# Kernel optimization log

Measured on AMD Instinct MI355X. Metric: run time of the kernel, lower is better.

The kernel has to match this reference:

```python
import jax, jax.numpy as jnp
from jax import lax
import numpy as np

B = 2
N_PER = 12000
TIMES = 16
C_IN = 4
# sparse_shape = grid_size[::-1] + [1,0,0], grid_size=[160,160,40]
S1 = (41, 160, 160)
S2 = (21, 80, 80)   # conv2: k3 s2 p1
S3 = (11, 40, 40)   # conv3: k3 s2 p1
S4 = (5, 20, 20)    # conv4: k3 s2 p(0,1,1)
SOUT = (2, 20, 20)  # conv_out: k(3,1,1) s(2,1,1) p0
# per-BN-layer channel counts, flattened into gamma/beta vectors
CH = [16, 16, 32, 32, 32, 64, 64, 64, 64, 64, 64, 128]
OFF = np.concatenate([[0], np.cumsum(CH)]).tolist()


def _downsample_coords(coords, in_shape, k, s, p):
    # spconv SparseConv3d output index rule: output j active iff some active
    # input x satisfies j*s - p <= x <= j*s - p + k - 1 within bounds.
    out_shape = np.array([(in_shape[i] + 2 * p[i] - k[i]) // s[i] + 1 for i in range(3)])
    b, xs = coords[:, :1], coords[:, 1:]
    s_arr = np.array(s)
    cand = []
    for o0 in range(k[0]):
        for o1 in range(k[1]):
            for o2 in range(k[2]):
                j = xs + np.array([p[0] - o0, p[1] - o1, p[2] - o2])
                ok = np.all(j % s_arr == 0, axis=1)
                jj = j // s_arr
                ok &= np.all((jj >= 0) & (jj < out_shape), axis=1)
                cand.append(np.concatenate([b[ok], jj[ok]], axis=1))
    return np.unique(np.concatenate(cand, axis=0), axis=0).astype(np.int32)


def _make_coords():
    rng = np.random.default_rng(0)
    ncell = S1[0] * S1[1] * S1[2]
    per = []
    for b in range(B):
        flat = rng.choice(ncell, size=N_PER, replace=False)
        z, y, x = np.unravel_index(flat, S1)
        per.append(np.stack([np.full(N_PER, b), z, y, x], axis=1))
    c1 = np.concatenate(per, axis=0).astype(np.int32)
    c2 = _downsample_coords(c1, S1, (3, 3, 3), (2, 2, 2), (1, 1, 1))
    c3 = _downsample_coords(c2, S2, (3, 3, 3), (2, 2, 2), (1, 1, 1))
    c4 = _downsample_coords(c3, S3, (3, 3, 3), (2, 2, 2), (0, 1, 1))
    c5 = _downsample_coords(c4, S4, (3, 1, 1), (2, 1, 1), (0, 0, 0))
    return c1, c2, c3, c4, c5


def _w(key, shape):
    fan_in = shape[0] * shape[1] * shape[2] * shape[3]
    return jax.random.normal(key, shape, jnp.float32) * np.float32(np.sqrt(2.0 / fan_in))


def setup_inputs():
    c1, c2, c3, c4, c5 = _make_coords()
    ks = jax.random.split(jax.random.key(0), 16)
    t = TIMES
    return {
        "voxel_features": jax.random.normal(ks[0], (c1.shape[0], C_IN), jnp.float32),
        "w_in": _w(ks[1], (3, 3, 3, C_IN, t)),
        "w1": _w(ks[2], (3, 3, 3, t, t)),
        "w2_0": _w(ks[3], (3, 3, 3, t, 2 * t)),
        "w2_1": _w(ks[4], (3, 3, 3, 2 * t, 2 * t)),
        "w2_2": _w(ks[5], (3, 3, 3, 2 * t, 2 * t)),
        "w3_0": _w(ks[6], (3, 3, 3, 2 * t, 4 * t)),
        "w3_1": _w(ks[7], (3, 3, 3, 4 * t, 4 * t)),
        "w3_2": _w(ks[8], (3, 3, 3, 4 * t, 4 * t)),
        "w4_0": _w(ks[9], (3, 3, 3, 4 * t, 4 * t)),
        "w4_1": _w(ks[10], (3, 3, 3, 4 * t, 4 * t)),
        "w4_2": _w(ks[11], (3, 3, 3, 4 * t, 4 * t)),
        "w_out": _w(ks[12], (3, 1, 1, 4 * t, 8 * t)),
        "gamma": 1.0 + 0.1 * jax.random.normal(ks[13], (sum(CH),), jnp.float32),
        "beta": 0.1 * jax.random.normal(ks[14], (sum(CH),), jnp.float32),
        "coords1": jnp.asarray(c1), "coords2": jnp.asarray(c2),
        "coords3": jnp.asarray(c3), "coords4": jnp.asarray(c4),
        "coords_out": jnp.asarray(c5),
    }


def _sp_conv(feats, in_coords, w, in_shape, out_coords, stride, padding):
    # spconv's rulebook gather->matmul->scatter over active sites computes the
    # same values as a dense conv on a zero-filled grid, read back only at the
    # active output coordinates (subm: out_coords == in_coords).
    dense = jnp.zeros((B,) + in_shape + (feats.shape[1],), feats.dtype)
    dense = dense.at[in_coords[:, 0], in_coords[:, 1], in_coords[:, 2], in_coords[:, 3]].set(feats)
    out = lax.conv_general_dilated(dense, w, window_strides=stride,
                                   padding=[(p, p) for p in padding],
                                   dimension_numbers=("NDHWC", "DHWIO", "NDHWC"))
    return out[out_coords[:, 0], out_coords[:, 1], out_coords[:, 2], out_coords[:, 3]]


def _bn_relu(x, g, b):
    # nn.BatchNorm1d(eps=1e-3) in training mode over the active voxels, + ReLU
    mu = jnp.mean(x, axis=0)
    var = jnp.mean(jnp.square(x - mu), axis=0)
    return jax.nn.relu((x - mu) * (g * lax.rsqrt(var + 1e-3)) + b)


def _forward(voxel_features, ws, gamma, beta, c1, c2, c3, c4, c5):
    layers = [
        (0, c1, S1, c1, (1, 1, 1), (1, 1, 1)),   # conv_input (subm, 4->16)
        (1, c1, S1, c1, (1, 1, 1), (1, 1, 1)),   # conv1 (subm)
        (2, c1, S1, c2, (2, 2, 2), (1, 1, 1)),   # conv2 spconv s2
        (3, c2, S2, c2, (1, 1, 1), (1, 1, 1)),
        (4, c2, S2, c2, (1, 1, 1), (1, 1, 1)),
        (5, c2, S2, c3, (2, 2, 2), (1, 1, 1)),   # conv3 spconv s2
        (6, c3, S3, c3, (1, 1, 1), (1, 1, 1)),
        (7, c3, S3, c3, (1, 1, 1), (1, 1, 1)),
        (8, c3, S3, c4, (2, 2, 2), (0, 1, 1)),   # conv4 spconv s2, pad (0,1,1)
        (9, c4, S4, c4, (1, 1, 1), (1, 1, 1)),
        (10, c4, S4, c4, (1, 1, 1), (1, 1, 1)),
        (11, c4, S4, c5, (2, 1, 1), (0, 0, 0)),  # conv_out k(3,1,1) s(2,1,1)
    ]
    x = voxel_features
    for i, ci, si, co, st, pd in layers:
        x = _sp_conv(x, ci, ws[i], si, co, st, pd)
        x = _bn_relu(x, gamma[OFF[i]:OFF[i + 1]], beta[OFF[i]:OFF[i + 1]])
    return x  # encoded_spconv_tensor features, [N_out, 8*times]


def reference(voxel_features, w_in, w1, w2_0, w2_1, w2_2, w3_0, w3_1, w3_2,
              w4_0, w4_1, w4_2, w_out, gamma, beta,
              coords1, coords2, coords3, coords4, coords_out):
    ws = [w_in, w1, w2_0, w2_1, w2_2, w3_0, w3_1, w3_2, w4_0, w4_1, w4_2, w_out]
    return _forward(voxel_features, ws, gamma, beta,
                    coords1, coords2, coords3, coords4, coords_out)
```

## Files before the change

kernel.cpp:

```cpp
#include <hip/hip_runtime.h>
#include <hip/hip_bf16.h>


typedef __attribute__((ext_vector_type(8))) short bf16x8;
typedef __attribute__((ext_vector_type(4))) short bf16x4s;
typedef __attribute__((ext_vector_type(4))) float f32x4;

typedef const __attribute__((address_space(1))) unsigned int* gas_ptr;
typedef __attribute__((address_space(3))) unsigned int* las_ptr;

__device__ __forceinline__ void dma16(const unsigned short* g, unsigned short* l) {
    __builtin_amdgcn_global_load_lds((gas_ptr)g, (las_ptr)l, 16, 0, 0);
}

__device__ __forceinline__ int xcd_swz(int wg, int nwg) {
    const int x = wg & 7, i = wg >> 3;
    const int q = nwg >> 3, r = nwg & 7;
    return (x < r ? x * (q + 1) : r * (q + 1) + (x - r) * q) + i;
}

__device__ inline unsigned short f2bf(float f) {
    unsigned u = __builtin_bit_cast(unsigned, f);
    u += 0x7FFFu + ((u >> 16) & 1u);
    return (unsigned short)(u >> 16);
}

struct ScatterArgs {
    const int* coords[4];
    int* grid[4];
    int n[4];
    int D[4], H[4], W[4];
};

__global__ __launch_bounds__(256) void scatter_grid_all(ScatterArgs a) {
    const int l = blockIdx.y;
    const int i = blockIdx.x * 256 + threadIdx.x;
    if (i >= a.n[l]) return;
    const int* c = a.coords[l] + 4 * i;
    a.grid[l][((c[0] * a.D[l] + c[1]) * a.H[l] + c[2]) * a.W[l] + c[3]] = i;
}

struct PrepArgs {
    const float* src[11];
    unsigned short* dst[11];
    int T[11], CIN[11], COUT[11], total[11];
};

__global__ __launch_bounds__(256) void prep_w_all(PrepArgs a) {
    const int l = blockIdx.y;
    const int i = blockIdx.x * 256 + threadIdx.x;
    if (i >= a.total[l]) return;
    const int COUT = a.COUT[l], CIN = a.CIN[l], T = a.T[l];
    const int co = i % COUT; const int r = i / COUT; const int ci = r % CIN; const int t = r / CIN;
    unsigned short v = (t < T) ? f2bf(a.src[l][i]) : (unsigned short)0;
    a.dst[l][((size_t)t * COUT + co) * CIN + ci] = v;
}

__global__ __launch_bounds__(256, 4) void sp_conv0(const float* __restrict__ fin,
                                                   const int* __restrict__ grid,
                                                   const int* __restrict__ oc, int n_out,
                                                   const float* __restrict__ w,
                                                   float* __restrict__ out,
                                                   int D, int H, int W) {
    const int c = threadIdx.x & 15;
    const int p = (blockIdx.x * 256 + threadIdx.x) >> 4;
    if (p >= n_out) return;
    const int b   = oc[4*p+0];
    const int iz0 = oc[4*p+1] - 1;
    const int iy0 = oc[4*p+2] - 1;
    const int ix0 = oc[4*p+3] - 1;
    const int* gb = grid + b * (D * H * W);
    float acc = 0.f;
    for (int kd = 0; kd < 3; ++kd) {
        const int iz = iz0 + kd;
        if ((unsigned)iz >= (unsigned)D) continue;
        for (int kh = 0; kh < 3; ++kh) {
            const int iy = iy0 + kh;
            if ((unsigned)iy >= (unsigned)H) continue;
            for (int kw = 0; kw < 3; ++kw) {
                const int ix = ix0 + kw;
                if ((unsigned)ix >= (unsigned)W) continue;
                const int idx = gb[(iz*H + iy)*W + ix];
                if (idx < 0) continue;
                const float4 v = *(const float4*)(fin + (size_t)idx * 4);
                const float* wp = w + (size_t)((kd*3 + kh)*3 + kw) * 64 + c;
                acc = fmaf(v.x, wp[0],  acc);
                acc = fmaf(v.y, wp[16], acc);
                acc = fmaf(v.z, wp[32], acc);
                acc = fmaf(v.w, wp[48], acc);
            }
        }
    }
    out[(size_t)p*16 + c] = acc;
}

template<int COUT>
__global__ __launch_bounds__(256, 4) void sp_conv_lds16(
    const unsigned short* __restrict__ fin, const int* __restrict__ grid,
    const int* __restrict__ oc, int n_out,
    const unsigned short* __restrict__ wt, float* __restrict__ out,
    float* __restrict__ stats,
    int D, int H, int W, int sz, int sy, int sx, int pz, int py, int px)
{
    constexpr int T  = 27;
    constexpr int BT = 4;
    constexpr int TP = 28;
    constexpr int NT = COUT/16;
    constexpr int NB = (COUT == 16) ? BT/2 : BT;

    __shared__ unsigned short Abuf[4*BT*16*16];
    __shared__ unsigned short Bbuf[BT*COUT*16];
    __shared__ float ls[2*COUT];

    const int l     = threadIdx.x & 63;
    const int w     = threadIdx.x >> 6;
    const int n     = l & 15;
    const int quad  = l >> 4;
    const int pbase = xcd_swz(blockIdx.x, gridDim.x) * 64 + w * 16;

    if (threadIdx.x < 2*COUT) ls[threadIdx.x] = 0.f;

    int idx[TP];
    if (quad == 0) {
        int pc = pbase + n;
        if (pc > n_out - 1) pc = n_out - 1;
        const int4 cc = ((const int4*)oc)[pc];
        const int* gb = grid + cc.x * (D * H * W);
        const int iz0 = cc.y * sz - pz;
        const int iy0 = cc.z * sy - py;
        const int ix0 = cc.w * sx - px;
#pragma unroll
        for (int tap = 0; tap < TP; ++tap) {
            const int te = tap < T ? tap : 0;
            const int kd = te/9, kr = te%9, kh = kr/3, kw = kr%3;
            const int iz = iz0 + kd, iy = iy0 + kh, ix = ix0 + kw;
            const bool ok = (tap < T) && (unsigned)iz < (unsigned)D &&
                            (unsigned)iy < (unsigned)H && (unsigned)ix < (unsigned)W;
            const int cz = iz < 0 ? 0 : (iz >= D ? D-1 : iz);
            const int cy = iy < 0 ? 0 : (iy >= H ? H-1 : iy);
            const int cx = ix < 0 ? 0 : (ix >= W ? W-1 : ix);
            const int g = gb[(cz*H + cy)*W + cx];
            idx[tap] = ok ? g : -1;
        }
    }

    f32x4 acc[NT];
#pragma unroll
    for (int t = 0; t < NT; ++t) acc[t] = (f32x4){0.f, 0.f, 0.f, 0.f};

    const int h  = l >> 5;
    const int m  = (l >> 1) & 15;
    const int ch = l & 1;

#pragma unroll
    for (int tb0 = 0; tb0 < TP; tb0 += BT) {
#pragma unroll
        for (int q = 0; q < BT/2; ++q) {
            const int v0 = __shfl(idx[tb0 + 2*q],     m);
            const int v1 = __shfl(idx[tb0 + 2*q + 1], m);
            const int row = h ? v1 : v0;
            const unsigned short* gp = fin + (ptrdiff_t)row*16 + ch*8;
            unsigned short* lp = Abuf + (w*BT + 2*q)*16*16;
            dma16(gp, lp);
        }
        for (int q = w; q < NB; q += 4) {
            if constexpr (COUT == 16) {
                const int tap = tb0 + 2*q + h;
                const int tw = tap < T ? tap : T;
                const unsigned short* gp = wt + ((size_t)tw*COUT + m)*16 + ch*8;
                unsigned short* lp = Bbuf + (2*q)*COUT*16;
                dma16(gp, lp);
            } else {
                const int tap = tb0 + q;
                const int tw = tap < T ? tap : T;
                const int r = l >> 1;
                const unsigned short* gp = wt + ((size_t)tw*COUT + r)*16 + ch*8;
                unsigned short* lp = Bbuf + q*COUT*16;
                dma16(gp, lp);
            }
        }
        __syncthreads();
#pragma unroll
        for (int jp = 0; jp < BT/2; ++jp) {
            const int ts = 2*jp + (quad >> 1);
            bf16x8 a = *(const bf16x8*)(Abuf + ((w*BT + ts)*16 + n)*16 + (quad & 1)*8);
#pragma unroll
            for (int t = 0; t < NT; ++t) {
                bf16x8 b = *(const bf16x8*)(Bbuf + (ts*COUT + t*16 + n)*16 + (quad & 1)*8);
                acc[t] = __builtin_amdgcn_mfma_f32_16x16x32_bf16(a, b, acc[t], 0, 0, 0);
            }
        }
        __syncthreads();
    }

#pragma unroll
    for (int t = 0; t < NT; ++t)
#pragma unroll
        for (int r = 0; r < 4; ++r) {
            const int p = pbase + quad*4 + r;
            if (p < n_out) out[(size_t)p * COUT + t*16 + n] = acc[t][r];
        }

#pragma unroll
    for (int t = 0; t < NT; ++t) {
        float s1 = 0.f, s2 = 0.f;
#pragma unroll
        for (int r = 0; r < 4; ++r) {
            const int p = pbase + quad*4 + r;
            if (p < n_out) { const float v = acc[t][r]; s1 += v; s2 += v*v; }
        }
        s1 += __shfl_xor(s1, 16); s2 += __shfl_xor(s2, 16);
        s1 += __shfl_xor(s1, 32); s2 += __shfl_xor(s2, 32);
        if (quad == 0) {
            atomicAdd(&ls[t*16 + n], s1);
            atomicAdd(&ls[COUT + t*16 + n], s2);
        }
    }
    __syncthreads();
    if (threadIdx.x < 2*COUT) atomicAdd(&stats[threadIdx.x], ls[threadIdx.x]);
}

template<int CIN, int COUT, int BT, int KD, int KH, int KW, int MB>
__global__ __launch_bounds__(256, MB) void sp_conv_lds(
    const unsigned short* __restrict__ fin, const int* __restrict__ grid,
    const int* __restrict__ oc, int n_out,
    const unsigned short* __restrict__ wt, float* __restrict__ out,
    float* __restrict__ stats,
    int D, int H, int W, int sz, int sy, int sx, int pz, int py, int px)
{
    constexpr int T    = KD*KH*KW;
    constexpr int TP   = ((T + BT - 1)/BT)*BT;
    constexpr int NT   = COUT/16;
    constexpr int S    = CIN/32;
    constexpr int LPR  = CIN/8;
    constexpr int RPD  = 64/LPR;
    constexpr int ADMA = 16/RPD;
    constexpr int BDMA = COUT/RPD;

    __shared__ unsigned short Abuf[4*BT*16*CIN];
    __shared__ unsigned short Bbuf[BT*COUT*CIN];
    __shared__ float ls[2*COUT];

    const int l     = threadIdx.x & 63;
    const int w     = threadIdx.x >> 6;
    const int n     = l & 15;
    const int quad  = l >> 4;
    const int pbase = xcd_swz(blockIdx.x, gridDim.x) * 64 + w * 16;

    if (threadIdx.x < 2*COUT) ls[threadIdx.x] = 0.f;

    int idx[TP];
    if (quad == 0) {
        int pc = pbase + n;
        if (pc > n_out - 1) pc = n_out - 1;
        const int4 cc = ((const int4*)oc)[pc];
        const int* gb = grid + cc.x * (D * H * W);
        const int iz0 = cc.y * sz - pz;
        const int iy0 = cc.z * sy - py;
        const int ix0 = cc.w * sx - px;
#pragma unroll
        for (int tap = 0; tap < TP; ++tap) {
            const int te = tap < T ? tap : 0;
            const int kd = te/(KH*KW), kr = te%(KH*KW), kh = kr/KW, kw = kr%KW;
            const int iz = iz0 + kd, iy = iy0 + kh, ix = ix0 + kw;
            const bool ok = (tap < T) && (unsigned)iz < (unsigned)D &&
                            (unsigned)iy < (unsigned)H && (unsigned)ix < (unsigned)W;
            const int cz = iz < 0 ? 0 : (iz >= D ? D-1 : iz);
            const int cy = iy < 0 ? 0 : (iy >= H ? H-1 : iy);
            const int cx = ix < 0 ? 0 : (ix >= W ? W-1 : ix);
            const int g = gb[(cz*H + cy)*W + cx];
            idx[tap] = ok ? g : -1;
        }
    }

    f32x4 acc[NT];
#pragma unroll
    for (int t = 0; t < NT; ++t) acc[t] = (f32x4){0.f, 0.f, 0.f, 0.f};

#pragma unroll
    for (int tb0 = 0; tb0 < TP; tb0 += BT) {
#pragma unroll
        for (int j = 0; j < BT; ++j) {
#pragma unroll
            for (int d = 0; d < ADMA; ++d) {
                const int m  = d*RPD + l/LPR;
                const int i0 = __shfl(idx[tb0+j], m);
                const int slot = (l % LPR) ^ (m % LPR);
                const unsigned short* gp = fin + (ptrdiff_t)i0*CIN + slot*8;
                unsigned short* lp = Abuf + ((w*BT + j)*16 + d*RPD)*CIN;
                dma16(gp, lp);
            }
        }
        for (int q = w; q < BT*BDMA; q += 4) {
            const int j = q / BDMA, d = q % BDMA;
            const int t = tb0 + j;
            const int tw = t < T ? t : T;
            const int r  = d*RPD + l/LPR;
            const int slot = (l % LPR) ^ (r % LPR);
            const unsigned short* gp = wt + ((size_t)tw*COUT + r)*CIN + slot*8;
            unsigned short* lp = Bbuf + (j*COUT + d*RPD)*CIN;
            dma16(gp, lp);
        }
        __syncthreads();
#pragma unroll
        for (int j = 0; j < BT; ++j) {
            const unsigned short* Aw = Abuf + (w*BT + j)*16*CIN;
            const unsigned short* Bw = Bbuf + j*COUT*CIN;
#pragma unroll
            for (int s = 0; s < S; ++s) {
                const int c = s*4 + quad;
                bf16x8 a = *(const bf16x8*)(Aw + n*CIN + ((c ^ (n % LPR)) * 8));
#pragma unroll
                for (int t = 0; t < NT; ++t) {
                    const int r = t*16 + n;
                    bf16x8 b = *(const bf16x8*)(Bw + r*CIN + ((c ^ (r % LPR)) * 8));
                    acc[t] = __builtin_amdgcn_mfma_f32_16x16x32_bf16(a, b, acc[t], 0, 0, 0);
                }
            }
        }
        __syncthreads();
    }

#pragma unroll
    for (int t = 0; t < NT; ++t)
#pragma unroll
        for (int r = 0; r < 4; ++r) {
            const int p = pbase + quad*4 + r;
            if (p < n_out) out[(size_t)p * COUT + t*16 + n] = acc[t][r];
        }

#pragma unroll
    for (int t = 0; t < NT; ++t) {
        float s1 = 0.f, s2 = 0.f;
#pragma unroll
        for (int r = 0; r < 4; ++r) {
            const int p = pbase + quad*4 + r;
            if (p < n_out) { const float v = acc[t][r]; s1 += v; s2 += v*v; }
        }
        s1 += __shfl_xor(s1, 16); s2 += __shfl_xor(s2, 16);
        s1 += __shfl_xor(s1, 32); s2 += __shfl_xor(s2, 32);
        if (quad == 0) {
            atomicAdd(&ls[t*16 + n], s1);
            atomicAdd(&ls[COUT + t*16 + n], s2);
        }
    }
    __syncthreads();
    if (threadIdx.x < 2*COUT) atomicAdd(&stats[threadIdx.x], ls[threadIdx.x]);
}

template<int CIN, int COUT, int BT, int MT, int MB>
__global__ __launch_bounds__(256, MB) void sp_conv_big(
    const unsigned short* __restrict__ fin, const int* __restrict__ grid,
    const int* __restrict__ oc, int n_out,
    const unsigned short* __restrict__ wt, float* __restrict__ out,
    float* __restrict__ stats,
    int D, int H, int W, int sz, int sy, int sx, int pz, int py, int px)
{
    constexpr int T    = 27;
    constexpr int TP   = ((T + BT - 1)/BT)*BT;
    constexpr int PPW  = MT*16;
    constexpr int NT   = COUT/16;
    constexpr int S    = CIN/32;
    constexpr int LPR  = CIN/8;
    constexpr int RPD  = 64/LPR;
    constexpr int ADMA = PPW/RPD;
    constexpr int BDMA = COUT/RPD;

    __shared__ unsigned short Abuf[4*BT*PPW*CIN];
    __shared__ unsigned short Bbuf[BT*COUT*CIN];
    __shared__ float ls[2*COUT];

    const int l     = threadIdx.x & 63;
    const int w     = threadIdx.x >> 6;
    const int n     = l & 15;
    const int quad  = l >> 4;
    const int wbase = xcd_swz(blockIdx.x, gridDim.x) * (4*PPW) + w * PPW;

    if (threadIdx.x < 2*COUT) ls[threadIdx.x] = 0.f;

    int idx[TP];
    {
        int pc = wbase + (l % PPW);
        if (pc > n_out - 1) pc = n_out - 1;
        const int4 cc = ((const int4*)oc)[pc];
        const int* gb = grid + cc.x * (D * H * W);
        const int iz0 = cc.y * sz - pz;
        const int iy0 = cc.z * sy - py;
        const int ix0 = cc.w * sx - px;
#pragma unroll
        for (int tap = 0; tap < TP; ++tap) {
            const int te = tap < T ? tap : 0;
            const int kd = te/9, kr = te%9, kh = kr/3, kw = kr%3;
            const int iz = iz0 + kd, iy = iy0 + kh, ix = ix0 + kw;
            const bool ok = (tap < T) && (unsigned)iz < (unsigned)D &&
                            (unsigned)iy < (unsigned)H && (unsigned)ix < (unsigned)W;
            const int cz = iz < 0 ? 0 : (iz >= D ? D-1 : iz);
            const int cy = iy < 0 ? 0 : (iy >= H ? H-1 : iy);
            const int cx = ix < 0 ? 0 : (ix >= W ? W-1 : ix);
            const int g = gb[(cz*H + cy)*W + cx];
            idx[tap] = ok ? g : -1;
        }
    }

    f32x4 acc[MT][NT];
#pragma unroll
    for (int mt = 0; mt < MT; ++mt)
#pragma unroll
        for (int t = 0; t < NT; ++t) acc[mt][t] = (f32x4){0.f, 0.f, 0.f, 0.f};

#pragma unroll
    for (int tb0 = 0; tb0 < TP; tb0 += BT) {
#pragma unroll
        for (int j = 0; j < BT; ++j) {
#pragma unroll
            for (int d = 0; d < ADMA; ++d) {
                const int r  = d*RPD + l/LPR;
                const int i0 = __shfl(idx[tb0+j], r);
                const int slot = (l % LPR) ^ (r % LPR);
                const unsigned short* gp = fin + (ptrdiff_t)i0*CIN + slot*8;
                unsigned short* lp = Abuf + ((w*BT + j)*PPW + d*RPD)*CIN;
                dma16(gp, lp);
            }
        }
        for (int q = w; q < BT*BDMA; q += 4) {
            const int j = q / BDMA, d = q % BDMA;
            const int t = tb0 + j;
            const int tw = t < T ? t : T;
            const int r  = d*RPD + l/LPR;
            const int slot = (l % LPR) ^ (r % LPR);
            const unsigned short* gp = wt + ((size_t)tw*COUT + r)*CIN + slot*8;
            unsigned short* lp = Bbuf + (j*COUT + d*RPD)*CIN;
            dma16(gp, lp);
        }
        __syncthreads();
#pragma unroll
        for (int j = 0; j < BT; ++j) {
            const unsigned short* Aw = Abuf + (w*BT + j)*PPW*CIN;
            const unsigned short* Bw = Bbuf + j*COUT*CIN;
#pragma unroll
            for (int s = 0; s < S; ++s) {
                const int c = s*4 + quad;
                bf16x8 bfr[NT];
#pragma unroll
                for (int t = 0; t < NT; ++t) {
                    const int r = t*16 + n;
                    bfr[t] = *(const bf16x8*)(Bw + r*CIN + ((c ^ (r % LPR)) * 8));
                }
#pragma unroll
                for (int mt = 0; mt < MT; ++mt) {
                    bf16x8 a = *(const bf16x8*)(Aw + (mt*16 + n)*CIN + ((c ^ (n % LPR)) * 8));
#pragma unroll
                    for (int t = 0; t < NT; ++t)
                        acc[mt][t] = __builtin_amdgcn_mfma_f32_16x16x32_bf16(a, bfr[t], acc[mt][t], 0, 0, 0);
                }
            }
        }
        __syncthreads();
    }

#pragma unroll
    for (int mt = 0; mt < MT; ++mt)
#pragma unroll
        for (int t = 0; t < NT; ++t)
#pragma unroll
            for (int r = 0; r < 4; ++r) {
                const int p = wbase + mt*16 + quad*4 + r;
                if (p < n_out) out[(size_t)p * COUT + t*16 + n] = acc[mt][t][r];
            }

#pragma unroll
    for (int t = 0; t < NT; ++t) {
        float s1 = 0.f, s2 = 0.f;
#pragma unroll
        for (int mt = 0; mt < MT; ++mt)
#pragma unroll
            for (int r = 0; r < 4; ++r) {
                const int p = wbase + mt*16 + quad*4 + r;
                if (p < n_out) { const float v = acc[mt][t][r]; s1 += v; s2 += v*v; }
            }
        s1 += __shfl_xor(s1, 16); s2 += __shfl_xor(s2, 16);
        s1 += __shfl_xor(s1, 32); s2 += __shfl_xor(s2, 32);
        if (quad == 0) {
            atomicAdd(&ls[t*16 + n], s1);
            atomicAdd(&ls[COUT + t*16 + n], s2);
        }
    }
    __syncthreads();
    if (threadIdx.x < 2*COUT) atomicAdd(&stats[threadIdx.x], ls[threadIdx.x]);
}

template<int C, int TZ, int TY, int TX, int BTW, int MB>
__global__ __launch_bounds__(256, MB) void sp_conv_dense(
    const unsigned short* __restrict__ dense, const int* __restrict__ grid,
    const unsigned short* __restrict__ wt, float* __restrict__ out,
    float* __restrict__ stats, const unsigned short* __restrict__ zrow,
    int D, int H, int W, int ZTn, int YTn, int XTn)
{
    constexpr int T   = 27;
    constexpr int HZ = TZ+2, HY = TY+2, HX = TX+2;
    constexpr int R   = HZ*HY*HX;
    constexpr int LPR = C/8;
    constexpr int RPD = 64/LPR;
    constexpr int RPI = 4*RPD;
    constexpr int NDMA = (R + RPI - 1)/RPI;
    constexpr int RPAD = NDMA*RPI;
    constexpr int M   = TZ*TY*TX;
    constexpr int WPW = M/4;
    constexpr int MT  = WPW/16;
    constexpr int NT  = C/16;
    constexpr int S   = C/32;
    constexpr int BDMA = C/RPD;

    __shared__ unsigned short Hbuf[RPAD*C];
    __shared__ unsigned short Bbuf[BTW*C*C];
    __shared__ float ls[2*C];

    const int l    = threadIdx.x & 63;
    const int w    = threadIdx.x >> 6;
    const int n    = l & 15;
    const int quad = l >> 4;

    int r1 = blockIdx.x;
    const int xt = r1 % XTn; r1 /= XTn;
    const int yt = r1 % YTn; r1 /= YTn;
    const int zt = r1 % ZTn; r1 /= ZTn;
    const int b  = r1;
    const int z0 = zt*TZ, y0 = yt*TY, x0 = xt*TX;
    const int* gb = grid + b * (D*H*W);
    const size_t dbase = (size_t)b * D*H*W;

    if (threadIdx.x < 2*C) ls[threadIdx.x] = 0.f;

#pragma unroll
    for (int d = 0; d < NDMA; ++d) {
        const int r0  = (d*4 + w)*RPD;
        const int row = r0 + l/LPR;
        const int slot = (l % LPR) ^ (row % LPR);
        const unsigned short* gp;
        if (row < R) {
            const int hz = row/(HY*HX);
            const int hy = (row/HX) % HY;
            const int hx = row % HX;
            const int gz = z0 - 1 + hz, gy = y0 - 1 + hy, gx = x0 - 1 + hx;
            const bool ok = (unsigned)gz < (unsigned)D && (unsigned)gy < (unsigned)H &&
                            (unsigned)gx < (unsigned)W;
            gp = ok ? dense + (dbase + (size_t)(gz*H + gy)*W + gx)*C + slot*8
                    : zrow + (l % LPR)*8;
        } else {
            gp = zrow + (l % LPR)*8;
        }
        dma16(gp, Hbuf + r0*C);
    }

    int prow[MT];
#pragma unroll
    for (int mt = 0; mt < MT; ++mt) {
        const int pos = w*WPW + mt*16 + n;
        const int dz = pos/(TY*TX), dy = (pos/TX)%TY, dx = pos%TX;
        prow[mt] = dz*(HY*HX) + dy*HX + dx;
    }

    f32x4 acc[MT][NT];
#pragma unroll
    for (int mt = 0; mt < MT; ++mt)
#pragma unroll
        for (int t = 0; t < NT; ++t) acc[mt][t] = (f32x4){0.f, 0.f, 0.f, 0.f};

#pragma unroll
    for (int batch = 0; batch < (T + BTW - 1)/BTW; ++batch) {
        const int tb0 = batch*BTW;
        const int nb  = (tb0 + BTW <= T) ? BTW : T - tb0;
        for (int q = w; q < nb*BDMA; q += 4) {
            const int j = q / BDMA, d = q % BDMA;
            const int tap = tb0 + j;
            const int rr  = d*RPD + l/LPR;
            const int slot = (l % LPR) ^ (rr % LPR);
            dma16(wt + ((size_t)tap*C + rr)*C + slot*8, Bbuf + (j*C + d*RPD)*C);
        }
        __syncthreads();
#pragma unroll
        for (int j = 0; j < nb; ++j) {
            const int tap = tb0 + j;
            const int kd = tap/9, kh = (tap/3)%3, kw = tap%3;
            const int toff = kd*(HY*HX) + kh*HX + kw;
#pragma unroll
            for (int s = 0; s < S; ++s) {
                const int c = s*4 + quad;
                bf16x8 bfr[NT];
#pragma unroll
                for (int t = 0; t < NT; ++t) {
                    const int rr = t*16 + n;
                    bfr[t] = *(const bf16x8*)(Bbuf + (j*C + rr)*C + ((c ^ (rr & (LPR-1)))*8));
                }
#pragma unroll
                for (int mt = 0; mt < MT; ++mt) {
                    const int arow = prow[mt] + toff;
                    bf16x8 a = *(const bf16x8*)(Hbuf + arow*C + ((c ^ (arow & (LPR-1)))*8));
#pragma unroll
                    for (int t = 0; t < NT; ++t)
                        acc[mt][t] = __builtin_amdgcn_mfma_f32_16x16x32_bf16(a, bfr[t], acc[mt][t], 0, 0, 0);
                }
            }
        }
        __syncthreads();
    }

    float s1[NT], s2[NT];
#pragma unroll
    for (int t = 0; t < NT; ++t) { s1[t] = 0.f; s2[t] = 0.f; }
#pragma unroll
    for (int mt = 0; mt < MT; ++mt) {
#pragma unroll
        for (int r = 0; r < 4; ++r) {
            const int pos = w*WPW + mt*16 + quad*4 + r;
            const int dz = pos/(TY*TX), dy = (pos/TX)%TY, dx = pos%TX;
            const int gz = z0 + dz, gy = y0 + dy, gx = x0 + dx;
            int p = -1;
            if (gz < D && gy < H && gx < W) p = gb[(gz*H + gy)*W + gx];
            if (p >= 0) {
#pragma unroll
                for (int t = 0; t < NT; ++t) {
                    const float v = acc[mt][t][r];
                    out[(size_t)p*C + t*16 + n] = v;
                    s1[t] += v; s2[t] += v*v;
                }
            }
        }
    }
#pragma unroll
    for (int t = 0; t < NT; ++t) {
        float a1 = s1[t], a2 = s2[t];
        a1 += __shfl_xor(a1, 16); a2 += __shfl_xor(a2, 16);
        a1 += __shfl_xor(a1, 32); a2 += __shfl_xor(a2, 32);
        if (quad == 0) {
            atomicAdd(&ls[t*16 + n], a1);
            atomicAdd(&ls[C + t*16 + n], a2);
        }
    }
    __syncthreads();
    if (threadIdx.x < 2*C) atomicAdd(&stats[threadIdx.x], ls[threadIdx.x]);
}

template<int C>
__global__ __launch_bounds__(256) void reduce_stats(const float* __restrict__ x, int nn,
                                                    float* __restrict__ stats)
{
    constexpr int R = 256 / C;
    __shared__ float s1[256];
    __shared__ float s2[256];
    const int c = threadIdx.x % C;
    const int r = threadIdx.x / C;
    float a1 = 0.f, a2 = 0.f;
    for (int i = blockIdx.x * R + r; i < nn; i += R * gridDim.x) {
        float v = x[(size_t)i*C + c];
        a1 += v;
        a2 += v * v;
    }
    s1[threadIdx.x] = a1;
    s2[threadIdx.x] = a2;
    __syncthreads();
    for (int off = 128; off >= C; off >>= 1) {
        if (threadIdx.x < off) {
            s1[threadIdx.x] += s1[threadIdx.x + off];
            s2[threadIdx.x] += s2[threadIdx.x + off];
        }
        __syncthreads();
    }
    if (threadIdx.x < C) {
        atomicAdd(&stats[c],     s1[threadIdx.x]);
        atomicAdd(&stats[C + c], s2[threadIdx.x]);
    }
}

__device__ inline void stv4(float* p, float4 v) { *(float4*)p = v; }
__device__ inline void stv4(unsigned short* p, float4 v) {
    bf16x4s o;
    o.x = (short)f2bf(v.x); o.y = (short)f2bf(v.y);
    o.z = (short)f2bf(v.z); o.w = (short)f2bf(v.w);
    *(bf16x4s*)p = o;
}

__device__ inline float4 bn_math(float4 xv, float4 s1, float4 s2, float4 gm, float4 bt,
                                 float inv_n) {
    float4 o;
    { float mu=s1.x*inv_n, var=s2.x*inv_n-mu*mu, g=gm.x*rsqrtf(var+1e-3f);
      float v=(xv.x-mu)*g+bt.x; o.x = v>0.f? v:0.f; }
    { float mu=s1.y*inv_n, var=s2.y*inv_n-mu*mu, g=gm.y*rsqrtf(var+1e-3f);
      float v=(xv.y-mu)*g+bt.y; o.y = v>0.f? v:0.f; }
    { float mu=s1.z*inv_n, var=s2.z*inv_n-mu*mu, g=gm.z*rsqrtf(var+1e-3f);
      float v=(xv.z-mu)*g+bt.z; o.z = v>0.f? v:0.f; }
    { float mu=s1.w*inv_n, var=s2.w*inv_n-mu*mu, g=gm.w*rsqrtf(var+1e-3f);
      float v=(xv.w-mu)*g+bt.w; o.w = v>0.f? v:0.f; }
    return o;
}

template<int C, typename OUT>
__global__ __launch_bounds__(256) void bn_relu_apply(const float* __restrict__ x,
                                                     OUT* __restrict__ y, int nn,
                                                     const float* __restrict__ stats,
                                                     const float* __restrict__ gamma,
                                                     const float* __restrict__ beta)
{
    const size_t q = (size_t)blockIdx.x * blockDim.x + threadIdx.x;
    if (q >= (size_t)nn * (C/4)) return;
    const int c = (int)(q % (size_t)(C/4)) * 4;
    const float4 o = bn_math(*(const float4*)(x + q*4),
                             *(const float4*)(stats + c), *(const float4*)(stats + C + c),
                             *(const float4*)(gamma + c), *(const float4*)(beta + c),
                             1.f / (float)nn);
    stv4(y + q*4, o);
}

template<int C>
__global__ __launch_bounds__(256) void bn_relu_apply_dense(const float* __restrict__ x,
                                                           unsigned short* __restrict__ dense,
                                                           int nn,
                                                           const float* __restrict__ stats,
                                                           const float* __restrict__ gamma,
                                                           const float* __restrict__ beta,
                                                           const int* __restrict__ coords,
                                                           int D, int H, int W)
{
    const size_t q = (size_t)blockIdx.x * blockDim.x + threadIdx.x;
    if (q >= (size_t)nn * (C/4)) return;
    const int c = (int)(q % (size_t)(C/4)) * 4;
    const int p = (int)(q / (size_t)(C/4));
    const float4 o = bn_math(*(const float4*)(x + q*4),
                             *(const float4*)(stats + c), *(const float4*)(stats + C + c),
                             *(const float4*)(gamma + c), *(const float4*)(beta + c),
                             1.f / (float)nn);
    const int4 cc = ((const int4*)coords)[p];
    const size_t cell = ((size_t)((cc.x*D + cc.y)*H + cc.z)*W + cc.w);
    stv4(dense + cell*C + c, o);
}

extern "C" void kernel_launch(void* const* d_in, const int* in_sizes, int n_in,
                              void* d_out, int out_size, void* d_ws, size_t ws_size,
                              hipStream_t stream) {
    const float* WPTR[12] = {
        (const float*)d_in[1], (const float*)d_in[2], (const float*)d_in[3],
        (const float*)d_in[4], (const float*)d_in[5], (const float*)d_in[6],
        (const float*)d_in[7], (const float*)d_in[8], (const float*)d_in[9],
        (const float*)d_in[10], (const float*)d_in[11], (const float*)d_in[12] };
    const float* vf    = (const float*)d_in[0];
    const float* gamma = (const float*)d_in[13];
    const float* beta  = (const float*)d_in[14];
    const int* c1 = (const int*)d_in[15];
    const int* c2 = (const int*)d_in[16];
    const int* c3 = (const int*)d_in[17];
    const int* c4 = (const int*)d_in[18];
    const int* c5 = (const int*)d_in[19];
    const int N1 = in_sizes[15] / 4;
    const int N2 = in_sizes[16] / 4;
    const int N3 = in_sizes[17] / 4;
    const int N4 = in_sizes[18] / 4;
    const int N5 = in_sizes[19] / 4;

    static const int LT[12]  = {27,27,27,27,27,27,27,27,27,27,27,3};
    static const int LCI[12] = {4,16,16,32,32,32,64,64,64,64,64,64};
    static const int LCO[12] = {16,16,32,32,32,64,64,64,64,64,64,128};

    const size_t G1 = (size_t)2*41*160*160;
    const size_t G2 = (size_t)2*21*80*80;
    const size_t G3 = (size_t)2*11*40*40;
    const size_t G4 = (size_t)2*5*20*20;
    int* grid1 = (int*)d_ws;
    int* grid2 = grid1 + G1;
    int* grid3 = grid2 + G2;
    int* grid4 = grid3 + G3;
    float* stats = (float*)(grid4 + G4);

    size_t maxE = (size_t)N1*16;
    if ((size_t)N2*32  > maxE) maxE = (size_t)N2*32;
    if ((size_t)N3*64  > maxE) maxE = (size_t)N3*64;
    if ((size_t)N4*64  > maxE) maxE = (size_t)N4*64;
    if ((size_t)N5*128 > maxE) maxE = (size_t)N5*128;
    maxE = (maxE + 7) & ~(size_t)7;

    float* raw = stats + 12*256;
    unsigned short* padA = (unsigned short*)(raw + maxE);
    unsigned short* fA   = padA + 128;
    unsigned short* padB = fA + maxE;
    unsigned short* fB   = padB + 128;
    unsigned short* wtb  = fB + maxE;
    size_t wtoff[12];
    size_t wtot = 0;
    {
        size_t o = 0;
        for (int i = 1; i < 12; ++i) {
            wtoff[i] = o;
            o += (size_t)(LT[i] + 1) * LCI[i] * LCO[i];
        }
        wtot = (o + 15) & ~(size_t)15;
    }
    unsigned short* dbuf = wtb + wtot;

    hipMemsetAsync(grid1, 0xFF, (G1+G2+G3+G4)*sizeof(int), stream);
    hipMemsetAsync(stats, 0, 12*256*sizeof(float), stream);
    hipMemsetAsync(padA, 0, 128*sizeof(unsigned short), stream);
    hipMemsetAsync(padB, 0, 128*sizeof(unsigned short), stream);

    {
        ScatterArgs sa;
        sa.coords[0]=c1; sa.coords[1]=c2; sa.coords[2]=c3; sa.coords[3]=c4;
        sa.grid[0]=grid1; sa.grid[1]=grid2; sa.grid[2]=grid3; sa.grid[3]=grid4;
        sa.n[0]=N1; sa.n[1]=N2; sa.n[2]=N3; sa.n[3]=N4;
        sa.D[0]=41; sa.H[0]=160; sa.W[0]=160;
        sa.D[1]=21; sa.H[1]= 80; sa.W[1]= 80;
        sa.D[2]=11; sa.H[2]= 40; sa.W[2]= 40;
        sa.D[3]= 5; sa.H[3]= 20; sa.W[3]= 20;
        int mx = N1; if (N2>mx) mx=N2; if (N3>mx) mx=N3; if (N4>mx) mx=N4;
        dim3 g((mx + 255)/256, 4);
        scatter_grid_all<<<g, 256, 0, stream>>>(sa);
    }
    {
        PrepArgs pa;
        int mx = 0;
        for (int i = 1; i < 12; ++i) {
            pa.src[i-1] = WPTR[i];
            pa.dst[i-1] = wtb + wtoff[i];
            pa.T[i-1] = LT[i]; pa.CIN[i-1] = LCI[i]; pa.COUT[i-1] = LCO[i];
            pa.total[i-1] = (LT[i]+1)*LCI[i]*LCO[i];
            if (pa.total[i-1] > mx) mx = pa.total[i-1];
        }
        dim3 g((mx + 255)/256, 11);
        prep_w_all<<<g, 256, 0, stream>>>(pa);
    }

    enum { GOFF_0 = 0, GOFF_1 = 16, GOFF_2 = 32, GOFF_3 = 64, GOFF_4 = 96, GOFF_5 = 128,
           GOFF_6 = 192, GOFF_7 = 256, GOFF_8 = 320, GOFF_9 = 384, GOFF_10 = 448, GOFF_11 = 512 };

#define APPLY(i, COUT, NP, FOUT_T, FOUT) \
    bn_relu_apply<COUT, FOUT_T><<<(((size_t)(NP)*(COUT)/4) + 255)/256, 256, 0, stream>>>( \
        raw, FOUT, NP, stats + (i)*256, gamma + GOFF_##i, beta + GOFF_##i);

#define APPLYD(i, C, NP, CC, D,H,W) \
    hipMemsetAsync(dbuf, 0, (size_t)2*(D)*(H)*(W)*(C)*2, stream); \
    bn_relu_apply_dense<C><<<(((size_t)(NP)*(C)/4) + 255)/256, 256, 0, stream>>>( \
        raw, dbuf, NP, stats + (i)*256, gamma + GOFF_##i, beta + GOFF_##i, CC, D,H,W);

    sp_conv0<<<((size_t)N1*16 + 255)/256, 256, 0, stream>>>(vf, grid1, c1, N1, WPTR[0], raw, 41,160,160);
    { int rb = (N1 + 15)/16; if (rb > 240) rb = 240;
      reduce_stats<16><<<rb, 256, 0, stream>>>(raw, N1, stats + 0*256); }
    APPLY(0, 16, N1, unsigned short, fA);

#define CONVS(i, COUT, FIN, GRD, OC, NP, D,H,W, SZ,SY,SX, PZ,PY,PX) \
    sp_conv_lds16<COUT><<<((NP)+63)/64, 256, 0, stream>>>( \
        FIN, GRD, OC, NP, wtb + wtoff[i], raw, stats + (i)*256, D,H,W, SZ,SY,SX, PZ,PY,PX);

#define CONVL(i, CIN, COUT, BT, MB, KD,KH,KW, FIN, GRD, OC, NP, D,H,W, SZ,SY,SX, PZ,PY,PX) \
    sp_conv_lds<CIN,COUT,BT,KD,KH,KW,MB><<<((NP)+63)/64, 256, 0, stream>>>( \
        FIN, GRD, OC, NP, wtb + wtoff[i], raw, stats + (i)*256, D,H,W, SZ,SY,SX, PZ,PY,PX);

#define CONVB(i, CIN, COUT, BT, MT, MB, FIN, GRD, OC, NP, D,H,W, SZ,SY,SX, PZ,PY,PX) \
    sp_conv_big<CIN,COUT,BT,MT,MB><<<((NP)+(64*(MT))-1)/(64*(MT)), 256, 0, stream>>>( \
        FIN, GRD, OC, NP, wtb + wtoff[i], raw, stats + (i)*256, D,H,W, SZ,SY,SX, PZ,PY,PX);

#define CONVD(i, C, TZ,TY,TX, BTW, MB, GRD, D,H,W) \
    { const int zt = ((D)+(TZ)-1)/(TZ), yt = ((H)+(TY)-1)/(TY), xt = ((W)+(TX)-1)/(TX); \
      sp_conv_dense<C,TZ,TY,TX,BTW,MB><<<2*zt*yt*xt, 256, 0, stream>>>( \
          dbuf, GRD, wtb + wtoff[i], raw, stats + (i)*256, padA, D,H,W, zt,yt,xt); }

    CONVS( 1, 16,       fA, grid1, c1, N1, 41,160,160, 1,1,1, 1,1,1); APPLY( 1, 16, N1, unsigned short, fB);
    CONVS( 2, 32,       fB, grid1, c2, N2, 41,160,160, 2,2,2, 1,1,1); APPLY( 2, 32, N2, unsigned short, fA);
    CONVB ( 3, 32, 32, 3, 4, 2, fA, grid2, c2, N2, 21, 80, 80, 1,1,1, 1,1,1); APPLY( 3, 32, N2, unsigned short, fB);
    CONVB ( 4, 32, 32, 3, 4, 2, fB, grid2, c2, N2, 21, 80, 80, 1,1,1, 1,1,1); APPLY( 4, 32, N2, unsigned short, fA);
    CONVB ( 5, 32, 64, 3, 2, 3, fA, grid2, c3, N3, 21, 80, 80, 2,2,2, 1,1,1); APPLYD( 5, 64, N3, c3, 11,40,40);
    CONVD ( 6, 64, 4,4,8, 3, 2, grid3, 11,40,40);                          APPLYD( 6, 64, N3, c3, 11,40,40);
    CONVD ( 7, 64, 4,4,8, 3, 2, grid3, 11,40,40);                          APPLY( 7, 64, N3, unsigned short, fB);
    CONVL ( 8, 64, 64, 9, 1, 3,3,3, fB, grid3, c4, N4, 11, 40, 40, 2,2,2, 0,1,1); APPLY( 8, 64, N4, unsigned short, fA);
    CONVL ( 9, 64, 64, 9, 1, 3,3,3, fA, grid4, c4, N4,  5, 20, 20, 1,1,1, 1,1,1); APPLY( 9, 64, N4, unsigned short, fB);
    CONVL (10, 64, 64, 9, 1, 3,3,3, fB, grid4, c4, N4,  5, 20, 20, 1,1,1, 1,1,1); APPLY(10, 64, N4, unsigned short, fA);
    CONVL (11, 64,128, 3, 2, 3,1,1, fA, grid4, c5, N5,  5, 20, 20, 2,1,1, 0,0,0); APPLY(11, 128, N5, float, (float*)d_out);
#undef CONVS
#undef CONVL
#undef CONVB
#undef CONVD
#undef APPLY
#undef APPLYD
}
```

Measured before the change: 382.6 us.

## Read conv weights directly from global memory instead of staging them in LDS

Removes the LDS weight buffers and their DMA staging loops from all four sparse and dense conv kernels. Each MFMA B operand is now loaded straight from global memory and relies on L1/L2 caching of the small weight tensors. The dense kernel drops its tap-batch loop and the barriers around it. The freed LDS lets the launch-bounds occupancy hint rise for several layers. The trade-off is more global-load latency on the MFMA inner loop, in exchange for less LDS traffic, fewer barriers and more waves per CU.

```diff
diff --git a/kernel.cpp b/kernel.cpp
--- a/kernel.cpp
+++ b/kernel.cpp
@@ -106,10 +106,8 @@
     constexpr int BT = 4;
     constexpr int TP = 28;
     constexpr int NT = COUT/16;
-    constexpr int NB = (COUT == 16) ? BT/2 : BT;
 
     __shared__ unsigned short Abuf[4*BT*16*16];
-    __shared__ unsigned short Bbuf[BT*COUT*16];
     __shared__ float ls[2*COUT];
 
     const int l     = threadIdx.x & 63;
@@ -163,30 +161,15 @@
             unsigned short* lp = Abuf + (w*BT + 2*q)*16*16;
             dma16(gp, lp);
         }
-        for (int q = w; q < NB; q += 4) {
-            if constexpr (COUT == 16) {
-                const int tap = tb0 + 2*q + h;
-                const int tw = tap < T ? tap : T;
-                const unsigned short* gp = wt + ((size_t)tw*COUT + m)*16 + ch*8;
-                unsigned short* lp = Bbuf + (2*q)*COUT*16;
-                dma16(gp, lp);
-            } else {
-                const int tap = tb0 + q;
-                const int tw = tap < T ? tap : T;
-                const int r = l >> 1;
-                const unsigned short* gp = wt + ((size_t)tw*COUT + r)*16 + ch*8;
-                unsigned short* lp = Bbuf + q*COUT*16;
-                dma16(gp, lp);
-            }
-        }
         __syncthreads();
 #pragma unroll
         for (int jp = 0; jp < BT/2; ++jp) {
-            const int ts = 2*jp + (quad >> 1);
+            const int ts  = 2*jp + (quad >> 1);
+            const int tap = tb0 + ts;
             bf16x8 a = *(const bf16x8*)(Abuf + ((w*BT + ts)*16 + n)*16 + (quad & 1)*8);
 #pragma unroll
             for (int t = 0; t < NT; ++t) {
-                bf16x8 b = *(const bf16x8*)(Bbuf + (ts*COUT + t*16 + n)*16 + (quad & 1)*8);
+                bf16x8 b = *(const bf16x8*)(wt + ((size_t)tap*COUT + t*16 + n)*16 + (quad & 1)*8);
                 acc[t] = __builtin_amdgcn_mfma_f32_16x16x32_bf16(a, b, acc[t], 0, 0, 0);
             }
         }
@@ -235,10 +218,8 @@
     constexpr int LPR  = CIN/8;
     constexpr int RPD  = 64/LPR;
     constexpr int ADMA = 16/RPD;
-    constexpr int BDMA = COUT/RPD;
 
     __shared__ unsigned short Abuf[4*BT*16*CIN];
-    __shared__ unsigned short Bbuf[BT*COUT*CIN];
     __shared__ float ls[2*COUT];
 
     const int l     = threadIdx.x & 63;
@@ -291,21 +272,12 @@
                 dma16(gp, lp);
             }
         }
-        for (int q = w; q < BT*BDMA; q += 4) {
-            const int j = q / BDMA, d = q % BDMA;
-            const int t = tb0 + j;
-            const int tw = t < T ? t : T;
-            const int r  = d*RPD + l/LPR;
-            const int slot = (l % LPR) ^ (r % LPR);
-            const unsigned short* gp = wt + ((size_t)tw*COUT + r)*CIN + slot*8;
-            unsigned short* lp = Bbuf + (j*COUT + d*RPD)*CIN;
-            dma16(gp, lp);
-        }
         __syncthreads();
 #pragma unroll
         for (int j = 0; j < BT; ++j) {
+            const int tap = tb0 + j;
+            const int tw  = tap < T ? tap : T;
             const unsigned short* Aw = Abuf + (w*BT + j)*16*CIN;
-            const unsigned short* Bw = Bbuf + j*COUT*CIN;
 #pragma unroll
             for (int s = 0; s < S; ++s) {
                 const int c = s*4 + quad;
@@ -313,7 +285,7 @@
 #pragma unroll
                 for (int t = 0; t < NT; ++t) {
                     const int r = t*16 + n;
-                    bf16x8 b = *(const bf16x8*)(Bw + r*CIN + ((c ^ (r % LPR)) * 8));
+                    bf16x8 b = *(const bf16x8*)(wt + ((size_t)tw*COUT + r)*CIN + c*8);
                     acc[t] = __builtin_amdgcn_mfma_f32_16x16x32_bf16(a, b, acc[t], 0, 0, 0);
                 }
             }
@@ -364,10 +336,8 @@
     constexpr int LPR  = CIN/8;
     constexpr int RPD  = 64/LPR;
     constexpr int ADMA = PPW/RPD;
-    constexpr int BDMA = COUT/RPD;
 
     __shared__ unsigned short Abuf[4*BT*PPW*CIN];
-    __shared__ unsigned short Bbuf[BT*COUT*CIN];
     __shared__ float ls[2*COUT];
 
     const int l     = threadIdx.x & 63;
@@ -422,21 +392,12 @@
                 dma16(gp, lp);
             }
         }
-        for (int q = w; q < BT*BDMA; q += 4) {
-            const int j = q / BDMA, d = q % BDMA;
-            const int t = tb0 + j;
-            const int tw = t < T ? t : T;
-            const int r  = d*RPD + l/LPR;
-            const int slot = (l % LPR) ^ (r % LPR);
-            const unsigned short* gp = wt + ((size_t)tw*COUT + r)*CIN + slot*8;
-            unsigned short* lp = Bbuf + (j*COUT + d*RPD)*CIN;
-            dma16(gp, lp);
-        }
         __syncthreads();
 #pragma unroll
         for (int j = 0; j < BT; ++j) {
+            const int tap = tb0 + j;
+            const int tw  = tap < T ? tap : T;
             const unsigned short* Aw = Abuf + (w*BT + j)*PPW*CIN;
-            const unsigned short* Bw = Bbuf + j*COUT*CIN;
 #pragma unroll
             for (int s = 0; s < S; ++s) {
                 const int c = s*4 + quad;
@@ -444,7 +405,7 @@
 #pragma unroll
                 for (int t = 0; t < NT; ++t) {
                     const int r = t*16 + n;
-                    bfr[t] = *(const bf16x8*)(Bw + r*CIN + ((c ^ (r % LPR)) * 8));
+                    bfr[t] = *(const bf16x8*)(wt + ((size_t)tw*COUT + r)*CIN + c*8);
                 }
 #pragma unroll
                 for (int mt = 0; mt < MT; ++mt) {
@@ -489,7 +450,7 @@
     if (threadIdx.x < 2*COUT) atomicAdd(&stats[threadIdx.x], ls[threadIdx.x]);
 }
 
-template<int C, int TZ, int TY, int TX, int BTW, int MB>
+template<int C, int TZ, int TY, int TX, int MB>
 __global__ __launch_bounds__(256, MB) void sp_conv_dense(
     const unsigned short* __restrict__ dense, const int* __restrict__ grid,
     const unsigned short* __restrict__ wt, float* __restrict__ out,
@@ -509,10 +470,8 @@
     constexpr int MT  = WPW/16;
     constexpr int NT  = C/16;
     constexpr int S   = C/32;
-    constexpr int BDMA = C/RPD;
 
     __shared__ unsigned short Hbuf[RPAD*C];
-    __shared__ unsigned short Bbuf[BTW*C*C];
     __shared__ float ls[2*C];
 
     const int l    = threadIdx.x & 63;
@@ -566,43 +525,30 @@
 #pragma unroll
         for (int t = 0; t < NT; ++t) acc[mt][t] = (f32x4){0.f, 0.f, 0.f, 0.f};
 
-#pragma unroll
-    for (int batch = 0; batch < (T + BTW - 1)/BTW; ++batch) {
-        const int tb0 = batch*BTW;
-        const int nb  = (tb0 + BTW <= T) ? BTW : T - tb0;
-        for (int q = w; q < nb*BDMA; q += 4) {
-            const int j = q / BDMA, d = q % BDMA;
-            const int tap = tb0 + j;
-            const int rr  = d*RPD + l/LPR;
-            const int slot = (l % LPR) ^ (rr % LPR);
-            dma16(wt + ((size_t)tap*C + rr)*C + slot*8, Bbuf + (j*C + d*RPD)*C);
-        }
-        __syncthreads();
-#pragma unroll
-        for (int j = 0; j < nb; ++j) {
-            const int tap = tb0 + j;
-            const int kd = tap/9, kh = (tap/3)%3, kw = tap%3;
-            const int toff = kd*(HY*HX) + kh*HX + kw;
-#pragma unroll
-            for (int s = 0; s < S; ++s) {
-                const int c = s*4 + quad;
-                bf16x8 bfr[NT];
-#pragma unroll
-                for (int t = 0; t < NT; ++t) {
-                    const int rr = t*16 + n;
-                    bfr[t] = *(const bf16x8*)(Bbuf + (j*C + rr)*C + ((c ^ (rr & (LPR-1)))*8));
-                }
-#pragma unroll
-                for (int mt = 0; mt < MT; ++mt) {
-                    const int arow = prow[mt] + toff;
-                    bf16x8 a = *(const bf16x8*)(Hbuf + arow*C + ((c ^ (arow & (LPR-1)))*8));
-#pragma unroll
-                    for (int t = 0; t < NT; ++t)
-                        acc[mt][t] = __builtin_amdgcn_mfma_f32_16x16x32_bf16(a, bfr[t], acc[mt][t], 0, 0, 0);
-                }
-            }
-        }
-        __syncthreads();
+    __syncthreads();
+
+#pragma unroll
+    for (int tap = 0; tap < T; ++tap) {
+        const int kd = tap/9, kh = (tap/3)%3, kw = tap%3;
+        const int toff = kd*(HY*HX) + kh*HX + kw;
+#pragma unroll
+        for (int s = 0; s < S; ++s) {
+            const int c = s*4 + quad;
+            bf16x8 bfr[NT];
+#pragma unroll
+            for (int t = 0; t < NT; ++t) {
+                const int rr = t*16 + n;
+                bfr[t] = *(const bf16x8*)(wt + ((size_t)tap*C + rr)*C + c*8);
+            }
+#pragma unroll
+            for (int mt = 0; mt < MT; ++mt) {
+                const int arow = prow[mt] + toff;
+                bf16x8 a = *(const bf16x8*)(Hbuf + arow*C + ((c ^ (arow & (LPR-1)))*8));
+#pragma unroll
+                for (int t = 0; t < NT; ++t)
+                    acc[mt][t] = __builtin_amdgcn_mfma_f32_16x16x32_bf16(a, bfr[t], acc[mt][t], 0, 0, 0);
+            }
+        }
     }
 
     float s1[NT], s2[NT];
@@ -856,21 +802,21 @@
     sp_conv_big<CIN,COUT,BT,MT,MB><<<((NP)+(64*(MT))-1)/(64*(MT)), 256, 0, stream>>>( \
         FIN, GRD, OC, NP, wtb + wtoff[i], raw, stats + (i)*256, D,H,W, SZ,SY,SX, PZ,PY,PX);
 
-#define CONVD(i, C, TZ,TY,TX, BTW, MB, GRD, D,H,W) \
+#define CONVD(i, C, TZ,TY,TX, MB, GRD, D,H,W) \
     { const int zt = ((D)+(TZ)-1)/(TZ), yt = ((H)+(TY)-1)/(TY), xt = ((W)+(TX)-1)/(TX); \
-      sp_conv_dense<C,TZ,TY,TX,BTW,MB><<<2*zt*yt*xt, 256, 0, stream>>>( \
+      sp_conv_dense<C,TZ,TY,TX,MB><<<2*zt*yt*xt, 256, 0, stream>>>( \
           dbuf, GRD, wtb + wtoff[i], raw, stats + (i)*256, padA, D,H,W, zt,yt,xt); }
 
     CONVS( 1, 16,       fA, grid1, c1, N1, 41,160,160, 1,1,1, 1,1,1); APPLY( 1, 16, N1, unsigned short, fB);
     CONVS( 2, 32,       fB, grid1, c2, N2, 41,160,160, 2,2,2, 1,1,1); APPLY( 2, 32, N2, unsigned short, fA);
-    CONVB ( 3, 32, 32, 3, 4, 2, fA, grid2, c2, N2, 21, 80, 80, 1,1,1, 1,1,1); APPLY( 3, 32, N2, unsigned short, fB);
-    CONVB ( 4, 32, 32, 3, 4, 2, fB, grid2, c2, N2, 21, 80, 80, 1,1,1, 1,1,1); APPLY( 4, 32, N2, unsigned short, fA);
+    CONVB ( 3, 32, 32, 3, 4, 3, fA, grid2, c2, N2, 21, 80, 80, 1,1,1, 1,1,1); APPLY( 3, 32, N2, unsigned short, fB);
+    CONVB ( 4, 32, 32, 3, 4, 3, fB, grid2, c2, N2, 21, 80, 80, 1,1,1, 1,1,1); APPLY( 4, 32, N2, unsigned short, fA);
     CONVB ( 5, 32, 64, 3, 2, 3, fA, grid2, c3, N3, 21, 80, 80, 2,2,2, 1,1,1); APPLYD( 5, 64, N3, c3, 11,40,40);
-    CONVD ( 6, 64, 4,4,8, 3, 2, grid3, 11,40,40);                          APPLYD( 6, 64, N3, c3, 11,40,40);
-    CONVD ( 7, 64, 4,4,8, 3, 2, grid3, 11,40,40);                          APPLY( 7, 64, N3, unsigned short, fB);
-    CONVL ( 8, 64, 64, 9, 1, 3,3,3, fB, grid3, c4, N4, 11, 40, 40, 2,2,2, 0,1,1); APPLY( 8, 64, N4, unsigned short, fA);
-    CONVL ( 9, 64, 64, 9, 1, 3,3,3, fA, grid4, c4, N4,  5, 20, 20, 1,1,1, 1,1,1); APPLY( 9, 64, N4, unsigned short, fB);
-    CONVL (10, 64, 64, 9, 1, 3,3,3, fB, grid4, c4, N4,  5, 20, 20, 1,1,1, 1,1,1); APPLY(10, 64, N4, unsigned short, fA);
+    CONVD ( 6, 64, 4,4,8, 3, grid3, 11,40,40);                          APPLYD( 6, 64, N3, c3, 11,40,40);
+    CONVD ( 7, 64, 4,4,8, 3, grid3, 11,40,40);                          APPLY( 7, 64, N3, unsigned short, fB);
+    CONVL ( 8, 64, 64, 9, 2, 3,3,3, fB, grid3, c4, N4, 11, 40, 40, 2,2,2, 0,1,1); APPLY( 8, 64, N4, unsigned short, fA);
+    CONVL ( 9, 64, 64, 9, 2, 3,3,3, fA, grid4, c4, N4,  5, 20, 20, 1,1,1, 1,1,1); APPLY( 9, 64, N4, unsigned short, fB);
+    CONVL (10, 64, 64, 9, 2, 3,3,3, fB, grid4, c4, N4,  5, 20, 20, 1,1,1, 1,1,1); APPLY(10, 64, N4, unsigned short, fA);
     CONVL (11, 64,128, 3, 2, 3,1,1, fA, grid4, c5, N5,  5, 20, 20, 2,1,1, 0,0,0); APPLY(11, 128, N5, float, (float*)d_out);
 #undef CONVS
 #undef CONVL
```

New measurement: 515.3 us. 34.7% more time.
